# Performance work log

Measured on AMD Instinct MI355X. Metric: run time of the kernel, lower is better.

The kernel has to match this reference:

```python
import math
import jax, jax.numpy as jnp
import numpy as np

B, C, H, W = 8, 256, 32, 32
NH, DK, DV = 8, 32, 32
EPS = 1e-6


def mish(x):
    return x * jnp.tanh(jax.nn.softplus(x))


def grouped_conv1x1(x, w, b, groups):
    # x: (B, Cin, N); w: (Cout, Cin//groups); b: (Cout,)
    Bb, Cin, N = x.shape
    Cout = w.shape[0]
    xg = x.reshape(Bb, groups, Cin // groups, N)
    wg = w.reshape(groups, Cout // groups, Cin // groups)
    y = jnp.einsum('bgin,goi->bgon', xg, wg).reshape(Bb, Cout, N)
    return y + b[None, :, None]


def conv_block(x, w, b, s, beta, groups):
    # 1x1 conv -> BatchNorm (eval: running mean 0 / var 1 => affine) -> Mish
    y = grouped_conv1x1(x, w, b, groups)
    y = s[None, :, None] * y + beta[None, :, None]
    return mish(y)


def setup_inputs() -> dict:
    key = jax.random.key(0)
    ks = jax.random.split(key, 8)
    inp = {
        'x': jax.random.normal(ks[0], (B, C, H, W), dtype=jnp.float32),
        'q_w': jax.random.normal(ks[1], (NH * DK, C // NH), dtype=jnp.float32) * 0.05,
        'q_b': jnp.zeros((NH * DK,), jnp.float32),
        'q_s': jnp.ones((NH * DK,), jnp.float32),
        'q_beta': jnp.zeros((NH * DK,), jnp.float32),
        'k_w': jax.random.normal(ks[2], (NH * DK, C // NH), dtype=jnp.float32) * 0.05,
        'k_b': jnp.zeros((NH * DK,), jnp.float32),
        'k_s': jnp.ones((NH * DK,), jnp.float32),
        'k_beta': jnp.zeros((NH * DK,), jnp.float32),
        'v_w': jax.random.normal(ks[3], (NH * DV, C // NH), dtype=jnp.float32) * 0.05,
        'v_b': jnp.zeros((NH * DV,), jnp.float32),
        'v_s': jnp.ones((NH * DV,), jnp.float32),
        'v_beta': jnp.zeros((NH * DV,), jnp.float32),
        'f_w': jax.random.normal(ks[4], (C, NH * DV), dtype=jnp.float32) * 0.05,
        'f_b': jnp.zeros((C,), jnp.float32),
        'f_s': jnp.ones((C,), jnp.float32),
        'f_beta': jnp.zeros((C,), jnp.float32),
    }
    return inp


def _forward(x, q_w, q_b, q_s, q_beta, k_w, k_b, k_s, k_beta,
             v_w, v_b, v_s, v_beta, f_w, f_b, f_s, f_beta):
    b, c, h, w = x.shape
    n = h * w
    temp = math.sqrt(c / NH)
    xf = x.reshape(b, c, n)

    q = conv_block(xf, q_w, q_b, q_s, q_beta, NH).reshape(b, NH, DK, n) / temp
    k = conv_block(xf, k_w, k_b, k_s, k_beta, NH).reshape(b, NH, DK, n)
    v = conv_block(xf, v_w, v_b, v_s, v_beta, NH).reshape(b, NH, DV, n)

    # cosine-distance attention (all heads vectorized); identical math to the
    # torch broadcast/repeat version but computed via normalized dot products.
    qn = jnp.sqrt(jnp.sum(q * q, axis=2))  # (b, nh, n)
    kn = jnp.sqrt(jnp.sum(k * k, axis=2))
    dot = jnp.einsum('bhdn,bhdm->bhnm', q, k)  # (b, nh, n, n)
    denom = jnp.maximum(qn[:, :, :, None] * kn[:, :, None, :], EPS)
    cos = jnp.clip(dot / denom, -1.0 + 1e-6, 1.0 - 1e-6)
    attn = jax.nn.softmax(1.0 - jnp.arccos(cos) / math.pi, axis=-1)

    # out[..., d, i] = sum_m v[..., d, m] * attn[..., i, m]
    out = jnp.einsum('bhdm,bhnm->bhdn', v, attn).reshape(b, NH * DV, n)

    y = conv_block(out, f_w, f_b, f_s, f_beta, 1).reshape(b, c, h, w) + x

    # extract_attn_map (no_grad in original)
    am = jnp.sum(jnp.mean(attn, axis=1), axis=1)  # (b, n)
    mn = jnp.min(am, axis=1, keepdims=True)
    mx = jnp.max(am, axis=1, keepdims=True)
    am = ((am - mn) / (mx - mn)).reshape(b, h, w)
    return y, jax.lax.stop_gradient(am)


def reference(x, q_w, q_b, q_s, q_beta, k_w, k_b, k_s, k_beta,
              v_w, v_b, v_s, v_beta, f_w, f_b, f_s, f_beta):
    return _forward(x, q_w, q_b, q_s, q_beta, k_w, k_b, k_s, k_beta,
                    v_w, v_b, v_s, v_beta, f_w, f_b, f_s, f_beta)
```

## Files before the change

### kernel.cpp

```cpp
#include <hip/hip_runtime.h>
#include <math.h>

#define B_   8
#define C_   256
#define NH_  8
#define N_   1024
#define LOG2E    1.4426950408889634f

typedef __attribute__((ext_vector_type(8))) short bf16x8;
typedef __attribute__((ext_vector_type(4))) float f32x4;
typedef __attribute__((ext_vector_type(2))) float f32x2;
typedef unsigned short u16;
typedef unsigned int u32;

#define AS1 __attribute__((address_space(1)))
#define AS3 __attribute__((address_space(3)))

__device__ __forceinline__ f32x4 mfma16(bf16x8 a, bf16x8 b, f32x4 c) {
    return __builtin_amdgcn_mfma_f32_16x16x32_bf16(a, b, c, 0, 0, 0);
}
__device__ __forceinline__ u32 bf16r(float x) {
    u32 b = __float_as_uint(x);
    return (b + 0x7fffu + ((b >> 16) & 1u)) >> 16;
}
__device__ __forceinline__ float mish_fast(float x) {
    float e  = __builtin_amdgcn_exp2f(fminf(x, 30.f) * LOG2E);
    float nm = e * (e + 2.f);
    return x * nm * __builtin_amdgcn_rcpf(nm + 2.f);
}
__device__ __forceinline__ f32x2 splat2(float v) { return (f32x2){v, v}; }
__device__ __forceinline__ f32x2 fexp_poly2(f32x2 c) {
    c = __builtin_elementwise_min(
            __builtin_elementwise_max(c, splat2(-0.999999f)), splat2(0.999999f));
    f32x2 r = __builtin_elementwise_fma(splat2(6.3713280f), c, splat2(1.7809920f));
    r = __builtin_elementwise_fma(r, c, splat2(-15.1427584f));
    r = __builtin_elementwise_fma(r, c, splat2(-3.7571968f));
    r = __builtin_elementwise_fma(r, c, splat2(13.1518784f));
    r = __builtin_elementwise_fma(r, c, splat2(2.8140000f));
    r = __builtin_elementwise_fma(r, c, splat2(-4.8903712f));
    r = __builtin_elementwise_fma(r, c, splat2(-0.8122592f));
    r = __builtin_elementwise_fma(r, c, splat2(0.8441120f));
    r = __builtin_elementwise_fma(r, c, splat2(0.1705120f));
    r = __builtin_elementwise_fma(r, c, splat2(0.4936541f));
    r = __builtin_elementwise_fma(r, c, splat2(1.6473155f));
    return r;
}

__global__ __launch_bounds__(256) void qkvpack_kernel(
    const float* __restrict__ x,
    const float* __restrict__ qw, const float* __restrict__ qb2,
    const float* __restrict__ qs, const float* __restrict__ qbeta,
    const float* __restrict__ kw, const float* __restrict__ kb2,
    const float* __restrict__ ks, const float* __restrict__ kbeta,
    const float* __restrict__ vw, const float* __restrict__ vb2,
    const float* __restrict__ vs, const float* __restrict__ vbeta,
    uint4* __restrict__ qpk, uint4* __restrict__ kpk, u16* __restrict__ vbf,
    const float* __restrict__ fw, u16* __restrict__ wbf)
{
    int blk = blockIdx.x;
    if (blk >= 768) {
        int id = (blk - 768) * 1024 + threadIdx.x;
#pragma unroll
        for (int j = 0; j < 4; ++j) { int p = id + j * 256; wbf[p] = (u16)bf16r(fw[p]); }
        return;
    }
    int type = blk >> 8;
    int sub = blk & 255;
    int nt = sub & 3, g = (sub >> 2) & 7, b = sub >> 5;
    int n = nt * 256 + threadIdx.x;
    int bh = b * 8 + g;
    const float* xp = x + ((size_t)b * C_ + g * 32) * N_ + n;
    float xv[32];
#pragma unroll
    for (int i = 0; i < 32; ++i) xv[i] = xp[(size_t)i * N_];

    const float *w, *bb, *sc, *bt;
    if (type == 0)      { w = qw; bb = qb2; sc = qs; bt = qbeta; }
    else if (type == 1) { w = kw; bb = kb2; sc = ks; bt = kbeta; }
    else                { w = vw; bb = vb2; sc = vs; bt = vbeta; }

    float y[32];
#pragma unroll
    for (int co = 0; co < 32; ++co) {
        int cg = g * 32 + co;
        float acc = 0.f;
#pragma unroll
        for (int i = 0; i < 32; ++i)
            acc = fmaf(xv[i], w[cg * 32 + i], acc);
        y[co] = mish_fast(sc[cg] * (acc + bb[cg]) + bt[cg]);
    }

    if (type == 2) {
#pragma unroll
        for (int co = 0; co < 32; ++co)
            vbf[((size_t)bh * 32 + co) * N_ + n] = (u16)bf16r(y[co]);
        return;
    }
    float s2 = 0.f;
#pragma unroll
    for (int d = 0; d < 32; ++d) s2 = fmaf(y[d], y[d], s2);
    float inv = __builtin_amdgcn_rsqf(fmaxf(s2, 1e-24f));
    u32 wp[16];
#pragma unroll
    for (int d = 0; d < 16; ++d)
        wp[d] = bf16r(y[2 * d] * inv) | (bf16r(y[2 * d + 1] * inv) << 16);
    uint4* dst = (type == 0 ? qpk : kpk) + ((size_t)bh * N_ + n) * 4;
#pragma unroll
    for (int j = 0; j < 4; ++j)
        dst[j] = make_uint4(wp[4 * j], wp[4 * j + 1], wp[4 * j + 2], wp[4 * j + 3]);
}

__global__ __launch_bounds__(256) void attn_kernel(
    const u16* __restrict__ qpk, const u16* __restrict__ kpk,
    const u16* __restrict__ vbf,
    u16* __restrict__ aout_bt, float* __restrict__ ampart)
{
    __shared__ __align__(16) u16 Ps[4][16 * 136];
    __shared__ __align__(16) float amW[N_];

    const int tid  = threadIdx.x;
    const int wave = tid >> 6, lane = tid & 63;
    const int l15 = lane & 15, lg = lane >> 4;
    const int blk = blockIdx.x;
    const int itile = blk & 15, bh = blk >> 4;
    const int h = bh & 7, bidx = bh >> 3;
    const int i0 = itile * 64;

    const char* ksrc = (const char*)(kpk + (size_t)bh * N_ * 32);
    const char* vsrc = (const char*)(vbf + (size_t)bh * 32 * N_);
    const char* qsrc = (const char*)(qpk + (size_t)bh * N_ * 32);

    for (int j = tid; j < N_; j += 256) amW[j] = 0.f;
    __syncthreads();

    bf16x8 aq = *(const bf16x8*)(qsrc + (size_t)(i0 + wave * 16 + l15) * 64 + lg * 16);

    const char* kfb = ksrc + l15 * 64 + lg * 16;
    const char* vfb = vsrc + l15 * 2048 + lg * 16;

    f32x2 rsL = {0.f, 0.f}, rsH = {0.f, 0.f};
#pragma unroll 8
    for (int t = 0; t < 64; ++t) {
        bf16x8 bk = *(const bf16x8*)(kfb + t * 1024);
        f32x4 cf = {0.f, 0.f, 0.f, 0.f};
        cf = mfma16(aq, bk, cf);
        rsL += fexp_poly2((f32x2){cf[0], cf[1]});
        rsH += fexp_poly2((f32x2){cf[2], cf[3]});
    }
    float rinv[4];
    {
        float rr[4] = {rsL.x, rsL.y, rsH.x, rsH.y};
#pragma unroll
        for (int r = 0; r < 4; ++r) {
            float s = rr[r];
            s += __shfl_xor(s, 1); s += __shfl_xor(s, 2);
            s += __shfl_xor(s, 4); s += __shfl_xor(s, 8);
            rinv[r] = __builtin_amdgcn_rcpf(s);
        }
    }
    f32x2 rinvL = {rinv[0], rinv[1]}, rinvH = {rinv[2], rinv[3]};

    f32x4 o0 = {0.f, 0.f, 0.f, 0.f}, o1 = {0.f, 0.f, 0.f, 0.f};
    char*       psw = (char*)&Ps[wave][0] + lg * 1088 + l15 * 2;
    const char* pab = (const char*)&Ps[wave][0] + l15 * 272 + lg * 16;

    for (int ch = 0; ch < 8; ++ch) {
        int m0 = ch * 128;
#pragma unroll
        for (int t = 0; t < 8; ++t) {
            bf16x8 bk = *(const bf16x8*)(kfb + (m0 + t * 16) * 64);
            f32x4 cf = {0.f, 0.f, 0.f, 0.f};
            cf = mfma16(aq, bk, cf);
            f32x2 fL = fexp_poly2((f32x2){cf[0], cf[1]});
            f32x2 fH = fexp_poly2((f32x2){cf[2], cf[3]});
            *(u16*)(psw + 0 * 272 + t * 32) = (u16)bf16r(fL.x);
            *(u16*)(psw + 1 * 272 + t * 32) = (u16)bf16r(fL.y);
            *(u16*)(psw + 2 * 272 + t * 32) = (u16)bf16r(fH.x);
            *(u16*)(psw + 3 * 272 + t * 32) = (u16)bf16r(fH.y);
            f32x2 cs2 = fL * rinvL;
            cs2 = __builtin_elementwise_fma(fH, rinvH, cs2);
            float csum = cs2.x + cs2.y;
            csum += __shfl_xor(csum, 16);
            csum += __shfl_xor(csum, 32);
            if (lane < 16) atomicAdd(&amW[m0 + t * 16 + l15], csum);
        }
        asm volatile("s_waitcnt lgkmcnt(0)" ::: "memory");
        __builtin_amdgcn_sched_barrier(0);
#pragma unroll
        for (int kss = 0; kss < 4; ++kss) {
            bf16x8 pa = *(const bf16x8*)(pab + kss * 64);
            const char* va = vfb + (m0 + kss * 32) * 2;
            bf16x8 v0 = *(const bf16x8*)va;
            bf16x8 v1 = *(const bf16x8*)(va + 32768);
            o0 = mfma16(pa, v0, o0);
            o1 = mfma16(pa, v1, o1);
        }
    }
    __syncthreads();

    {
        u16* oT = (u16*)Ps;
#pragma unroll
        for (int r = 0; r < 4; ++r) {
            int irow = wave * 16 + lg * 4 + r;
            oT[irow * 40 + l15]      = (u16)bf16r(o0[r] * rinv[r]);
            oT[irow * 40 + 16 + l15] = (u16)bf16r(o1[r] * rinv[r]);
        }
    }
    __syncthreads();
    {
        const u16* oT = (const u16*)Ps;
        int row = tid >> 2, c4 = tid & 3;
        uint4 val = *(const uint4*)((const char*)oT + row * 80 + c4 * 16);
        int n = i0 + row;
        int g = h * 4 + c4;
        size_t dst = ((size_t)(bidx * N_ + n) << 9) + ((size_t)((g ^ (row & 7)) << 4));
        *(uint4*)((char*)aout_bt + dst) = val;
    }
#pragma unroll
    for (int j2 = 0; j2 < 4; ++j2)
        ampart[(size_t)blk * N_ + tid + 256 * j2] = amW[tid + 256 * j2];
}

__global__ __launch_bounds__(256) void fconv_kernel(
    const u16* __restrict__ aout_bt, const u16* __restrict__ wbf,
    const float* __restrict__ x,
    const float* __restrict__ fs, const float* __restrict__ fb,
    const float* __restrict__ fbeta, float* __restrict__ y,
    const float* __restrict__ ampart, float* __restrict__ outAm)
{
    __shared__ __align__(16) u16 As[32 * 256];
    __shared__ float rmn[256], rmx[256];
    const int tid = threadIdx.x;

    if (blockIdx.x >= 256) {
        int b = blockIdx.x - 256;
        const float* base = ampart + (size_t)b * 128 * N_;
        float s[4] = {0.f, 0.f, 0.f, 0.f};
        for (int p = 0; p < 128; ++p) {
#pragma unroll
            for (int c2 = 0; c2 < 4; ++c2)
                s[c2] += base[(size_t)p * N_ + tid + 256 * c2];
        }
        float mn = fminf(fminf(s[0], s[1]), fminf(s[2], s[3]));
        float mx = fmaxf(fmaxf(s[0], s[1]), fmaxf(s[2], s[3]));
        rmn[tid] = mn; rmx[tid] = mx;
        __syncthreads();
        for (int off = 128; off >= 1; off >>= 1) {
            if (tid < off) {
                rmn[tid] = fminf(rmn[tid], rmn[tid + off]);
                rmx[tid] = fmaxf(rmx[tid], rmx[tid + off]);
            }
            __syncthreads();
        }
        mn = rmn[0]; mx = rmx[0];
        float inv = 1.f / (mx - mn);
#pragma unroll
        for (int c2 = 0; c2 < 4; ++c2)
            outAm[(size_t)b * N_ + tid + 256 * c2] = (s[c2] - mn) * inv;
        return;
    }

    const int wave = tid >> 6, lane = tid & 63;
    const int l15 = lane & 15, lg = lane >> 4;
    const int b  = blockIdx.x >> 5;
    const int n0 = (blockIdx.x & 31) * 32;

    const char* asrc = (const char*)aout_bt + ((size_t)(b * N_ + n0) << 9);
#pragma unroll
    for (int p = 0; p < 4; ++p) {
        int g = p * 256 + wave * 64 + lane;
        __builtin_amdgcn_global_load_lds(
            (const AS1 void*)(asrc + g * 16),
            (AS3 void*)((char*)As + ((p * 256 + wave * 64) << 4)), 16, 0, 0);
    }
    __syncthreads();

    f32x4 acc[4][2];
#pragma unroll
    for (int f = 0; f < 4; ++f)
#pragma unroll
        for (int fn = 0; fn < 2; ++fn) acc[f][fn] = (f32x4){0.f, 0.f, 0.f, 0.f};

    const int cobase = wave * 64;
#pragma unroll
    for (int kk = 0; kk < 8; ++kk) {
        bf16x8 af[2];
#pragma unroll
        for (int fn = 0; fn < 2; ++fn) {
            int nf = fn * 16 + l15;
            af[fn] = *(const bf16x8*)((const char*)As + nf * 512 +
                                      (((kk * 4 + lg) ^ (nf & 7)) << 4));
        }
#pragma unroll
        for (int f = 0; f < 4; ++f) {
            bf16x8 wf = *(const bf16x8*)(wbf + (size_t)(cobase + f * 16 + l15) * 256 + kk * 32 + lg * 8);
            acc[f][0] = mfma16(wf, af[0], acc[f][0]);
            acc[f][1] = mfma16(wf, af[1], acc[f][1]);
        }
    }

#pragma unroll
    for (int f = 0; f < 4; ++f) {
#pragma unroll
        for (int r = 0; r < 4; ++r) {
            int co = cobase + f * 16 + lg * 4 + r;
            float sc = fs[co], bb = fb[co], bt = fbeta[co];
#pragma unroll
            for (int fn = 0; fn < 2; ++fn) {
                int n = n0 + fn * 16 + l15;
                size_t oid = ((size_t)(b * C_ + co) << 10) + n;
                y[oid] = mish_fast(sc * (acc[f][fn][r] + bb) + bt) + x[oid];
            }
        }
    }
}

extern "C" void kernel_launch(void* const* d_in, const int* in_sizes, int n_in,
                              void* d_out, int out_size, void* d_ws, size_t ws_size,
                              hipStream_t stream)
{
    const float* x     = (const float*)d_in[0];
    const float* q_w   = (const float*)d_in[1];
    const float* q_b   = (const float*)d_in[2];
    const float* q_s   = (const float*)d_in[3];
    const float* q_be  = (const float*)d_in[4];
    const float* k_w   = (const float*)d_in[5];
    const float* k_b   = (const float*)d_in[6];
    const float* k_s   = (const float*)d_in[7];
    const float* k_be  = (const float*)d_in[8];
    const float* v_w   = (const float*)d_in[9];
    const float* v_b   = (const float*)d_in[10];
    const float* v_s   = (const float*)d_in[11];
    const float* v_be  = (const float*)d_in[12];
    const float* f_w   = (const float*)d_in[13];
    const float* f_b   = (const float*)d_in[14];
    const float* f_s   = (const float*)d_in[15];
    const float* f_be  = (const float*)d_in[16];

    float* y_out  = (float*)d_out;
    float* am_out = (float*)d_out + (size_t)B_ * C_ * N_;

    char* w = (char*)d_ws;
    u16*   qpk     = (u16*)w;    w += (size_t)B_ * NH_ * N_ * 64;
    u16*   kpk     = (u16*)w;    w += (size_t)B_ * NH_ * N_ * 64;
    u16*   vbf     = (u16*)w;    w += (size_t)B_ * C_ * N_ * 2;
    u16*   aout_bt = (u16*)w;    w += (size_t)B_ * N_ * C_ * 2;
    float* ampart  = (float*)w;  w += (size_t)B_ * NH_ * 16 * N_ * 4;
    u16*   wbf     = (u16*)w;

    qkvpack_kernel<<<832, 256, 0, stream>>>(
        x, q_w, q_b, q_s, q_be, k_w, k_b, k_s, k_be,
        v_w, v_b, v_s, v_be, (uint4*)qpk, (uint4*)kpk, vbf, f_w, wbf);

    attn_kernel<<<B_ * NH_ * 16, 256, 0, stream>>>(
        qpk, kpk, vbf, aout_bt, ampart);

    fconv_kernel<<<264, 256, 0, stream>>>(
        aout_bt, wbf, x, f_s, f_b, f_be, y_out, ampart, am_out);
}
```

Before: 119.4 us.

## Stage K/V chunks through LDS with register prefetch and drop LDS atomics

The attention kernel now loads K and V cooperatively into shared-memory chunk buffers, using register prefetch of the next chunk and barriers, instead of having each wave read K/V fragments directly from global memory. The per-block shared attention-map accumulator with atomics is replaced by direct per-wave stores to a larger partial buffer, so the final reduction now sums four times as many partials. The exp polynomial is rewritten in even/odd (Estrin-like) form to shorten its dependency chain, and block indices are swizzled so consecutive blocks run on different heads. The added barriers and the larger ampart traffic and reduction are the costs of this change.

```diff
diff --git a/kernel.cpp b/kernel.cpp
--- a/kernel.cpp
+++ b/kernel.cpp
@@ -32,18 +32,18 @@
 __device__ __forceinline__ f32x2 fexp_poly2(f32x2 c) {
     c = __builtin_elementwise_min(
             __builtin_elementwise_max(c, splat2(-0.999999f)), splat2(0.999999f));
-    f32x2 r = __builtin_elementwise_fma(splat2(6.3713280f), c, splat2(1.7809920f));
-    r = __builtin_elementwise_fma(r, c, splat2(-15.1427584f));
-    r = __builtin_elementwise_fma(r, c, splat2(-3.7571968f));
-    r = __builtin_elementwise_fma(r, c, splat2(13.1518784f));
-    r = __builtin_elementwise_fma(r, c, splat2(2.8140000f));
-    r = __builtin_elementwise_fma(r, c, splat2(-4.8903712f));
-    r = __builtin_elementwise_fma(r, c, splat2(-0.8122592f));
-    r = __builtin_elementwise_fma(r, c, splat2(0.8441120f));
-    r = __builtin_elementwise_fma(r, c, splat2(0.1705120f));
-    r = __builtin_elementwise_fma(r, c, splat2(0.4936541f));
-    r = __builtin_elementwise_fma(r, c, splat2(1.6473155f));
-    return r;
+    f32x2 u = c * c;
+    f32x2 p = __builtin_elementwise_fma(splat2(1.7809920f), u, splat2(-3.7571968f));
+    f32x2 q = __builtin_elementwise_fma(splat2(6.3713280f), u, splat2(-15.1427584f));
+    p = __builtin_elementwise_fma(p, u, splat2(2.8140000f));
+    q = __builtin_elementwise_fma(q, u, splat2(13.1518784f));
+    p = __builtin_elementwise_fma(p, u, splat2(-0.8122592f));
+    q = __builtin_elementwise_fma(q, u, splat2(-4.8903712f));
+    p = __builtin_elementwise_fma(p, u, splat2(0.1705120f));
+    q = __builtin_elementwise_fma(q, u, splat2(0.8441120f));
+    p = __builtin_elementwise_fma(p, u, splat2(1.6473155f));
+    q = __builtin_elementwise_fma(q, u, splat2(0.4936541f));
+    return __builtin_elementwise_fma(c, q, p);
 }
 
 __global__ __launch_bounds__(256) void qkvpack_kernel(
@@ -115,14 +115,15 @@
     const u16* __restrict__ vbf,
     u16* __restrict__ aout_bt, float* __restrict__ ampart)
 {
+    __shared__ __align__(16) u16 Kc[512 * 8];
+    __shared__ __align__(16) u16 Vc[512 * 8];
     __shared__ __align__(16) u16 Ps[4][16 * 136];
-    __shared__ __align__(16) float amW[N_];
 
     const int tid  = threadIdx.x;
     const int wave = tid >> 6, lane = tid & 63;
     const int l15 = lane & 15, lg = lane >> 4;
-    const int blk = blockIdx.x;
-    const int itile = blk & 15, bh = blk >> 4;
+    const int swz = (blockIdx.x & 7) * 128 + (blockIdx.x >> 3);
+    const int itile = swz & 15, bh = swz >> 4;
     const int h = bh & 7, bidx = bh >> 3;
     const int i0 = itile * 64;
 
@@ -130,22 +131,45 @@
     const char* vsrc = (const char*)(vbf + (size_t)bh * 32 * N_);
     const char* qsrc = (const char*)(qpk + (size_t)bh * N_ * 32);
 
-    for (int j = tid; j < N_; j += 256) amW[j] = 0.f;
-    __syncthreads();
+    const int kj0 = tid >> 7, km0g = tid & 127;
+    const int kj1 = (256 + tid) >> 7, km1g = (256 + tid) & 127;
+    const int vd0 = tid >> 4, vg0 = tid & 15;
+    const int vd1 = (256 + tid) >> 4, vg1 = (256 + tid) & 15;
+    const size_t koff0 = (size_t)km0g * 64 + kj0 * 16;
+    const size_t koff1 = (size_t)km1g * 64 + kj1 * 16;
+    const size_t voff0 = (size_t)vd0 * 2048 + ((vg0 ^ (vd0 & 7)) << 4);
+    const size_t voff1 = (size_t)vd1 * 2048 + ((vg1 ^ (vd1 & 7)) << 4);
 
     bf16x8 aq = *(const bf16x8*)(qsrc + (size_t)(i0 + wave * 16 + l15) * 64 + lg * 16);
 
-    const char* kfb = ksrc + l15 * 64 + lg * 16;
-    const char* vfb = vsrc + l15 * 2048 + lg * 16;
-
+    const char* kfb = (const char*)Kc + lg * 2048 + l15 * 16;
+
+    uint4 kreg0 = *(const uint4*)(ksrc + koff0);
+    uint4 kreg1 = *(const uint4*)(ksrc + koff1);
     f32x2 rsL = {0.f, 0.f}, rsH = {0.f, 0.f};
-#pragma unroll 8
-    for (int t = 0; t < 64; ++t) {
-        bf16x8 bk = *(const bf16x8*)(kfb + t * 1024);
-        f32x4 cf = {0.f, 0.f, 0.f, 0.f};
-        cf = mfma16(aq, bk, cf);
-        rsL += fexp_poly2((f32x2){cf[0], cf[1]});
-        rsH += fexp_poly2((f32x2){cf[2], cf[3]});
+    for (int ch = 0; ch < 8; ++ch) {
+        *(uint4*)((char*)Kc + tid * 16)         = kreg0;
+        *(uint4*)((char*)Kc + (256 + tid) * 16) = kreg1;
+        if (ch < 7) {
+            kreg0 = *(const uint4*)(ksrc + (size_t)(ch + 1) * 8192 + koff0);
+            kreg1 = *(const uint4*)(ksrc + (size_t)(ch + 1) * 8192 + koff1);
+        }
+        asm volatile("s_waitcnt lgkmcnt(0)" ::: "memory");
+        __builtin_amdgcn_sched_barrier(0);
+        __builtin_amdgcn_s_barrier();
+        __builtin_amdgcn_sched_barrier(0);
+#pragma unroll
+        for (int t = 0; t < 8; ++t) {
+            bf16x8 bk = *(const bf16x8*)(kfb + t * 256);
+            f32x4 cf = {0.f, 0.f, 0.f, 0.f};
+            cf = mfma16(aq, bk, cf);
+            rsL += fexp_poly2((f32x2){cf[0], cf[1]});
+            rsH += fexp_poly2((f32x2){cf[2], cf[3]});
+        }
+        asm volatile("s_waitcnt lgkmcnt(0)" ::: "memory");
+        __builtin_amdgcn_sched_barrier(0);
+        __builtin_amdgcn_s_barrier();
+        __builtin_amdgcn_sched_barrier(0);
     }
     float rinv[4];
     {
@@ -163,12 +187,35 @@
     f32x4 o0 = {0.f, 0.f, 0.f, 0.f}, o1 = {0.f, 0.f, 0.f, 0.f};
     char*       psw = (char*)&Ps[wave][0] + lg * 1088 + l15 * 2;
     const char* pab = (const char*)&Ps[wave][0] + l15 * 272 + lg * 16;
+    const char* vfb = (const char*)Vc + l15 * 256;
+    const int   vkey = l15 & 7;
+    float* amrow = ampart + (size_t)(swz * 4 + wave) * N_;
+
+    kreg0 = *(const uint4*)(ksrc + koff0);
+    kreg1 = *(const uint4*)(ksrc + koff1);
+    uint4 vreg0 = *(const uint4*)(vsrc + voff0);
+    uint4 vreg1 = *(const uint4*)(vsrc + voff1);
 
     for (int ch = 0; ch < 8; ++ch) {
         int m0 = ch * 128;
+        *(uint4*)((char*)Kc + tid * 16)         = kreg0;
+        *(uint4*)((char*)Kc + (256 + tid) * 16) = kreg1;
+        *(uint4*)((char*)Vc + tid * 16)         = vreg0;
+        *(uint4*)((char*)Vc + (256 + tid) * 16) = vreg1;
+        if (ch < 7) {
+            kreg0 = *(const uint4*)(ksrc + (size_t)(ch + 1) * 8192 + koff0);
+            kreg1 = *(const uint4*)(ksrc + (size_t)(ch + 1) * 8192 + koff1);
+            vreg0 = *(const uint4*)(vsrc + (size_t)(ch + 1) * 256 + voff0);
+            vreg1 = *(const uint4*)(vsrc + (size_t)(ch + 1) * 256 + voff1);
+        }
+        asm volatile("s_waitcnt lgkmcnt(0)" ::: "memory");
+        __builtin_amdgcn_sched_barrier(0);
+        __builtin_amdgcn_s_barrier();
+        __builtin_amdgcn_sched_barrier(0);
+
 #pragma unroll
         for (int t = 0; t < 8; ++t) {
-            bf16x8 bk = *(const bf16x8*)(kfb + (m0 + t * 16) * 64);
+            bf16x8 bk = *(const bf16x8*)(kfb + t * 256);
             f32x4 cf = {0.f, 0.f, 0.f, 0.f};
             cf = mfma16(aq, bk, cf);
             f32x2 fL = fexp_poly2((f32x2){cf[0], cf[1]});
@@ -182,21 +229,24 @@
             float csum = cs2.x + cs2.y;
             csum += __shfl_xor(csum, 16);
             csum += __shfl_xor(csum, 32);
-            if (lane < 16) atomicAdd(&amW[m0 + t * 16 + l15], csum);
+            if (lane < 16) amrow[m0 + t * 16 + l15] = csum;
         }
         asm volatile("s_waitcnt lgkmcnt(0)" ::: "memory");
         __builtin_amdgcn_sched_barrier(0);
 #pragma unroll
         for (int kss = 0; kss < 4; ++kss) {
             bf16x8 pa = *(const bf16x8*)(pab + kss * 64);
-            const char* va = vfb + (m0 + kss * 32) * 2;
+            const char* va = vfb + (((kss * 4 + lg) ^ vkey) << 4);
             bf16x8 v0 = *(const bf16x8*)va;
-            bf16x8 v1 = *(const bf16x8*)(va + 32768);
+            bf16x8 v1 = *(const bf16x8*)(va + 4096);
             o0 = mfma16(pa, v0, o0);
             o1 = mfma16(pa, v1, o1);
         }
-    }
-    __syncthreads();
+        asm volatile("s_waitcnt lgkmcnt(0)" ::: "memory");
+        __builtin_amdgcn_sched_barrier(0);
+        __builtin_amdgcn_s_barrier();
+        __builtin_amdgcn_sched_barrier(0);
+    }
 
     {
         u16* oT = (u16*)Ps;
@@ -217,9 +267,6 @@
         size_t dst = ((size_t)(bidx * N_ + n) << 9) + ((size_t)((g ^ (row & 7)) << 4));
         *(uint4*)((char*)aout_bt + dst) = val;
     }
-#pragma unroll
-    for (int j2 = 0; j2 < 4; ++j2)
-        ampart[(size_t)blk * N_ + tid + 256 * j2] = amW[tid + 256 * j2];
 }
 
 __global__ __launch_bounds__(256) void fconv_kernel(
@@ -235,9 +282,9 @@
 
     if (blockIdx.x >= 256) {
         int b = blockIdx.x - 256;
-        const float* base = ampart + (size_t)b * 128 * N_;
+        const float* base = ampart + (size_t)b * 512 * N_;
         float s[4] = {0.f, 0.f, 0.f, 0.f};
-        for (int p = 0; p < 128; ++p) {
+        for (int p = 0; p < 512; ++p) {
 #pragma unroll
             for (int c2 = 0; c2 < 4; ++c2)
                 s[c2] += base[(size_t)p * N_ + tid + 256 * c2];
@@ -346,7 +393,7 @@
     u16*   kpk     = (u16*)w;    w += (size_t)B_ * NH_ * N_ * 64;
     u16*   vbf     = (u16*)w;    w += (size_t)B_ * C_ * N_ * 2;
     u16*   aout_bt = (u16*)w;    w += (size_t)B_ * N_ * C_ * 2;
-    float* ampart  = (float*)w;  w += (size_t)B_ * NH_ * 16 * N_ * 4;
+    float* ampart  = (float*)w;  w += (size_t)B_ * NH_ * 16 * 4 * N_ * 4;
     u16*   wbf     = (u16*)w;
 
     qkvpack_kernel<<<832, 256, 0, stream>>>(
```

Measured after the change: 121.6 us. About the same (+1.8%).
